# Kernel tuning notes

Measured on AMD Instinct MI355X. Metric: run time of the kernel, lower is better.

## Reference

```python
import jax, jax.numpy as jnp
import numpy as np

N_CELL = 400000
N_NET = 100000
E_PIN = 1600000
E2 = 400000
RAW_C = 8; RAW_N = 8; RAW_P = 8
HC = 64; HN = 64; HP = 16


def setup_inputs() -> dict:
    key = jax.random.key(0)
    ks = jax.random.split(key, 32)
    f32 = jnp.float32

    def lin(k, fan_in, fan_out):
        k1, k2 = jax.random.split(k)
        W = jax.random.normal(k1, (fan_in, fan_out), f32) / np.float32(np.sqrt(fan_in))
        b = jax.random.normal(k2, (fan_out,), f32) * 0.01
        return W, b

    inp = {}
    inp['cell_feat'] = jax.random.normal(ks[0], (N_CELL, RAW_C), f32)
    inp['net_feat'] = jax.random.normal(ks[1], (N_NET, RAW_N), f32)
    inp['pin_feat'] = jax.random.normal(ks[2], (E_PIN, RAW_P), f32)
    inp['cell_size'] = jax.random.uniform(ks[3], (N_CELL, 2), f32)
    inp['W_cell'], inp['b_cell'] = lin(ks[4], RAW_C + 2 * RAW_N, HC)
    inp['W_net'], inp['b_net'] = lin(ks[5], RAW_N + 2 * RAW_C, HN)
    inp['W_pin'], inp['b_pin'] = lin(ks[6], RAW_P, HP)
    inp['W_ew'], inp['b_ew'] = lin(ks[7], HP, 1)
    inp['W_self'] = jax.random.normal(ks[8], (HC, HC), f32) / np.float32(np.sqrt(HC))
    inp['W_neigh'] = jax.random.normal(ks[9], (HN, HC), f32) / np.float32(np.sqrt(HN))
    inp['b_sage'] = jax.random.normal(ks[10], (HC,), f32) * 0.01
    inp['W_dis'], inp['b_dis'] = lin(ks[11], 2 * HC + HN, 1)
    inp['W_def'], inp['b_def'] = lin(ks[12], 3 * HC + 2 * HN, 1)
    # 'pins' edges: cell -> net; 'pinned' is the reverse (net -> cell), same edge set
    inp['pins_src'] = jax.random.randint(ks[13], (E_PIN,), 0, N_CELL, jnp.int32)
    inp['pins_dst'] = jax.random.randint(ks[14], (E_PIN,), 0, N_NET, jnp.int32)
    # points-to family: all four etypes share the same 'fathers' ordering (asserted in torch)
    inp['fathers'] = jax.random.randint(ks[15], (E2,), 0, N_CELL, jnp.int32)
    inp['sons'] = jax.random.randint(ks[16], (E2,), 0, N_CELL, jnp.int32)
    inp['grandfathers'] = jax.random.randint(ks[17], (E2,), 0, N_CELL, jnp.int32)
    inp['fs_nets'] = jax.random.randint(ks[18], (E2,), 0, N_NET, jnp.int32)
    inp['gf_nets'] = jax.random.randint(ks[19], (E2,), 0, N_NET, jnp.int32)
    return inp


def _seg_mean_max(x, idx, n):
    # DGL fn.mean / fn.max semantics: zero-in-degree nodes get 0
    cnt = jax.ops.segment_sum(jnp.ones((idx.shape[0], 1), x.dtype), idx, num_segments=n)
    mean = jax.ops.segment_sum(x, idx, num_segments=n) / jnp.maximum(cnt, 1.0)
    mx = jax.ops.segment_max(x, idx, num_segments=n)
    mx = jnp.where(cnt > 0, mx, 0.0)
    return mean, mx, cnt


def reference(cell_feat, net_feat, pin_feat, cell_size,
              W_cell, b_cell, W_net, b_net, W_pin, b_pin, W_ew, b_ew,
              W_self, W_neigh, b_sage, W_dis, b_dis, W_def, b_def,
              pins_src, pins_dst, fathers, sons, grandfathers, fs_nets, gf_nets):
    n_cell = cell_feat.shape[0]
    n_net = net_feat.shape[0]
    # update_all over 'pins' (cell->net) and 'pinned' (net->cell): mean & max of src feats
    net_mean, net_max, _ = _seg_mean_max(cell_feat[pins_src], pins_dst, n_net)
    cell_mean, cell_max, cell_cnt = _seg_mean_max(net_feat[pins_dst], pins_src, n_cell)
    hc = jnp.tanh(jnp.concatenate([cell_feat, cell_mean, cell_max], axis=-1) @ W_cell + b_cell)
    hn = jnp.tanh(jnp.concatenate([net_feat, net_mean, net_max], axis=-1) @ W_net + b_net)
    hp = jnp.tanh(pin_feat @ W_pin + b_pin)
    # single pass: SAGEConv(mean) on 'pinned' with scalar edge weights
    ew = jnp.tanh(hp @ W_ew + b_ew)  # [E_PIN, 1]
    msg = hn[pins_dst] * ew          # src of 'pinned' edge = net
    h_neigh = jax.ops.segment_sum(msg, pins_src, num_segments=n_cell) / jnp.maximum(cell_cnt, 1.0)
    hidden_cell = hc @ W_self + h_neigh @ W_neigh + b_sage  # [N_CELL, HC]
    # gather-based edge readouts
    pair = jnp.concatenate([hidden_cell[fathers], hidden_cell[sons], hn[fs_nets]], axis=-1)
    ext = jnp.concatenate([hidden_cell[grandfathers], hidden_cell[fathers], hidden_cell[sons],
                           hn[gf_nets], hn[fs_nets]], axis=-1)
    edge_dis_ = jnp.exp(-2.0 + 15.0 * jnp.tanh(pair @ W_dis + b_dis)).reshape(-1)
    edge_deflect = jnp.tanh(ext @ W_def + b_def).reshape(-1) * (2.0 * jnp.pi)
    bound = (cell_size[fathers] + cell_size[sons]) * 0.5  # [E2, 2]
    edge_dis = edge_dis_ + jnp.min(bound, axis=1)
    return edge_dis, edge_deflect
```

## Files before the change

kernel.cpp:

```cpp
#include <hip/hip_runtime.h>
#include <math.h>

#define N_CELL 400000
#define N_NET  100000
#define E_PIN  1600000
#define E2     400000


__global__ void __launch_bounds__(256) k_hist(
    const int* __restrict__ src, const int* __restrict__ dst,
    int* __restrict__ cell_deg, int* __restrict__ net_deg)
{
    int e = blockIdx.x * 256 + threadIdx.x;
    if (e >= E_PIN) return;
    atomicAdd(&net_deg[dst[e]], 1);
    atomicAdd(&cell_deg[src[e]], 1);
}

__global__ void __launch_bounds__(256) k_alloc(
    const int* __restrict__ deg, int* __restrict__ ptr, int* __restrict__ cur,
    int* __restrict__ cursor, int n)
{
    __shared__ int s[256];
    __shared__ int base;
    int tid = threadIdx.x;
    int i = blockIdx.x * 256 + tid;
    int d = (i < n) ? deg[i] : 0;
    int v = d;
    s[tid] = v;
    __syncthreads();
    for (int o = 1; o < 256; o <<= 1) {
        int t = (tid >= o) ? s[tid - o] : 0;
        __syncthreads();
        v += t;
        s[tid] = v;
        __syncthreads();
    }
    if (tid == 255) base = atomicAdd(cursor, v);
    __syncthreads();
    if (i < n) {
        int p = base + v - d;
        ptr[i] = p;
        cur[i] = p;
    }
}

__global__ void __launch_bounds__(256) k_fill(
    const int* __restrict__ src, const int* __restrict__ dst,
    int* __restrict__ net_cur, int* __restrict__ cell_cur,
    int* __restrict__ csr_net_cell, int* __restrict__ csr_cell_net,
    int* __restrict__ edge_slot)
{
    int e = blockIdx.x * 256 + threadIdx.x;
    if (e >= E_PIN) return;
    int s = src[e], d = dst[e];
    int p = atomicAdd(&net_cur[d], 1);
    csr_net_cell[p] = s;
    int q = atomicAdd(&cell_cur[s], 1);
    csr_cell_net[q] = d;
    edge_slot[e] = q;
}

__global__ void __launch_bounds__(256) k_ew(
    const float* __restrict__ pin_feat,
    const float* __restrict__ W_pin, const float* __restrict__ b_pin,
    const float* __restrict__ W_ew, const float* __restrict__ b_ew,
    const int* __restrict__ edge_slot,
    float* __restrict__ ew_csr)
{
    __shared__ float Wp[8 * 16];
    __shared__ float bp[16];
    __shared__ float We[16];
    __shared__ float be_s;
    int tid = threadIdx.x;
    if (tid < 128) Wp[tid] = W_pin[tid];
    if (tid < 16) { bp[tid] = b_pin[tid]; We[tid] = W_ew[tid]; }
    if (tid == 0) be_s = b_ew[0];
    __syncthreads();
    int e = blockIdx.x * 256 + tid;
    if (e >= E_PIN) return;
    float p[8];
    #pragma unroll
    for (int k = 0; k < 8; ++k) p[k] = pin_feat[e * 8 + k];
    float acc = be_s;
    #pragma unroll
    for (int j = 0; j < 16; ++j) {
        float h = bp[j];
        #pragma unroll
        for (int k = 0; k < 8; ++k) h += p[k] * Wp[k * 16 + j];
        acc += tanhf(h) * We[j];
    }
    ew_csr[edge_slot[e]] = tanhf(acc);
}

__global__ void __launch_bounds__(256) k_net(
    const float* __restrict__ net_feat, const float* __restrict__ cell_feat,
    const int* __restrict__ net_ptr, const int* __restrict__ net_deg,
    const int* __restrict__ csr_cell,
    const float* __restrict__ W_net, const float* __restrict__ b_net,
    const float* __restrict__ W_neigh,
    const float* __restrict__ W_dis, const float* __restrict__ W_def,
    float* __restrict__ hnW, float* __restrict__ npack)
{
    __shared__ float smem[11648];
    float* xs24 = smem;
    float* Ws24 = smem + 1600;
    float* HN   = smem + 3136;
    float* Wn   = smem + 7296;
    float* Wd3  = smem + 11392;
    float* bs   = smem + 11584;

    int tid = threadIdx.x;
    int w = tid >> 6, l = tid & 63;
    int tile = blockIdx.x * 64;

    for (int i = tid; i < 1536; i += 256) Ws24[i] = W_net[i];
    for (int i = tid; i < 4096; i += 256) Wn[i] = W_neigh[i];
    if (tid < 192) Wd3[tid] = (tid < 64) ? W_dis[128 + tid] : W_def[128 + tid];
    if (tid < 64) bs[tid] = b_net[tid];

    int g = l >> 3, k = l & 7;
    #pragma unroll
    for (int p = 0; p < 2; ++p) {
        int rl = p * 32 + w * 8 + g;
        int row = tile + rl;
        int base = 0, deg = 0;
        if (row < N_NET) { base = net_ptr[row]; deg = net_deg[row]; }
        float sum = 0.0f, mx = -INFINITY;
        for (int j = 0; j < deg; ++j) {
            int idx = csr_cell[base + j];
            float v = cell_feat[idx * 8 + k];
            sum += v;
            mx = fmaxf(mx, v);
        }
        float inv = (deg > 0) ? 1.0f / (float)deg : 1.0f;
        float sf = (row < N_NET) ? net_feat[row * 8 + k] : 0.0f;
        xs24[rl * 25 + k] = sf;
        xs24[rl * 25 + 8 + k] = sum * inv;
        xs24[rl * 25 + 16 + k] = (deg > 0) ? mx : 0.0f;
    }
    __syncthreads();

    int rg = l >> 2, cc = l & 3, c0 = w * 16 + cc * 4;
    {
        float acc[4][4];
        #pragma unroll
        for (int i = 0; i < 4; ++i) {
            float4 b4 = *(const float4*)&bs[c0];
            acc[i][0] = b4.x; acc[i][1] = b4.y; acc[i][2] = b4.z; acc[i][3] = b4.w;
        }
        for (int kk = 0; kk < 24; ++kk) {
            float4 wv = *(const float4*)&Ws24[kk * 64 + c0];
            #pragma unroll
            for (int i = 0; i < 4; ++i) {
                float x = xs24[(rg * 4 + i) * 25 + kk];
                acc[i][0] += x * wv.x; acc[i][1] += x * wv.y;
                acc[i][2] += x * wv.z; acc[i][3] += x * wv.w;
            }
        }
        #pragma unroll
        for (int i = 0; i < 4; ++i)
            #pragma unroll
            for (int j = 0; j < 4; ++j)
                HN[(rg * 4 + i) * 65 + c0 + j] = tanhf(acc[i][j]);
    }
    __syncthreads();

    {
        float acc[4][4];
        #pragma unroll
        for (int i = 0; i < 4; ++i)
            #pragma unroll
            for (int j = 0; j < 4; ++j) acc[i][j] = 0.0f;
        for (int kk = 0; kk < 64; ++kk) {
            float4 wv = *(const float4*)&Wn[kk * 64 + c0];
            #pragma unroll
            for (int i = 0; i < 4; ++i) {
                float x = HN[(rg * 4 + i) * 65 + kk];
                acc[i][0] += x * wv.x; acc[i][1] += x * wv.y;
                acc[i][2] += x * wv.z; acc[i][3] += x * wv.w;
            }
        }
        #pragma unroll
        for (int i = 0; i < 4; ++i) {
            int row = tile + rg * 4 + i;
            if (row < N_NET)
                *(float4*)&hnW[(size_t)row * 64 + c0] =
                    make_float4(acc[i][0], acc[i][1], acc[i][2], acc[i][3]);
        }
    }

    {
        int row = tid & 63, d = tid >> 6;
        float a = 0.0f;
        if (d < 3)
            for (int kk = 0; kk < 64; ++kk) a += HN[row * 65 + kk] * Wd3[d * 64 + kk];
        int grow = tile + row;
        if (grow < N_NET) npack[(size_t)grow * 4 + d] = (d < 3) ? a : 0.0f;
    }
}

__global__ void __launch_bounds__(256) k_cell(
    const float* __restrict__ cell_feat, const float* __restrict__ net_feat,
    const float* __restrict__ cell_size,
    const int* __restrict__ cell_ptr, const int* __restrict__ cell_deg,
    const int* __restrict__ csr_net, const float* __restrict__ ew_csr,
    const float* __restrict__ hnW,
    const float* __restrict__ W_cell, const float* __restrict__ b_cell,
    const float* __restrict__ W_self, const float* __restrict__ b_sage,
    const float* __restrict__ W_dis, const float* __restrict__ W_def,
    float* __restrict__ cellpack)
{
    __shared__ float smem[12864];
    float* xs24 = smem;
    float* Ws24 = smem + 1600;
    float* XN   = smem;
    float* X    = smem + 4160;
    float* Wsf  = smem + 8320;
    float* Wd5  = smem + 12416;
    float* bs24 = smem + 12736;
    float* bsg  = smem + 12800;

    int tid = threadIdx.x;
    int w = tid >> 6, l = tid & 63;
    int tile = blockIdx.x * 64;

    for (int i = tid; i < 1536; i += 256) Ws24[i] = W_cell[i];
    for (int i = tid; i < 4096; i += 256) Wsf[i] = W_self[i];
    if (tid < 64) { bs24[tid] = b_cell[tid]; bsg[tid] = b_sage[tid]; }
    { int i = tid; if (i < 320) Wd5[i] = (i < 128) ? W_dis[i] : W_def[i - 128]; }

    int g = l >> 3, k = l & 7;
    float4 xa[2], xb[2];
    #pragma unroll
    for (int p = 0; p < 2; ++p) {
        int rl = p * 32 + w * 8 + g;
        int row = tile + rl;
        int base = cell_ptr[row], deg = cell_deg[row];
        float sum = 0.0f, mx = -INFINITY;
        float4 a0 = make_float4(0, 0, 0, 0), a1 = make_float4(0, 0, 0, 0);
        for (int j = 0; j < deg; ++j) {
            int slot = base + j;
            int net = csr_net[slot];
            float wt = ew_csr[slot];
            float v = net_feat[net * 8 + k];
            sum += v;
            mx = fmaxf(mx, v);
            const float4* hp = (const float4*)(hnW + (size_t)net * 64 + k * 8);
            float4 u = hp[0], u2 = hp[1];
            a0.x += wt * u.x;  a0.y += wt * u.y;  a0.z += wt * u.z;  a0.w += wt * u.w;
            a1.x += wt * u2.x; a1.y += wt * u2.y; a1.z += wt * u2.z; a1.w += wt * u2.w;
        }
        float inv = (deg > 0) ? 1.0f / (float)deg : 1.0f;
        xs24[rl * 25 + k] = cell_feat[row * 8 + k];
        xs24[rl * 25 + 8 + k] = sum * inv;
        xs24[rl * 25 + 16 + k] = (deg > 0) ? mx : 0.0f;
        xa[p] = make_float4(a0.x * inv, a0.y * inv, a0.z * inv, a0.w * inv);
        xb[p] = make_float4(a1.x * inv, a1.y * inv, a1.z * inv, a1.w * inv);
    }
    __syncthreads();

    int rg = l >> 2, cc = l & 3, c0 = w * 16 + cc * 4;
    {
        float acc[4][4];
        #pragma unroll
        for (int i = 0; i < 4; ++i) {
            float4 b4 = *(const float4*)&bs24[c0];
            acc[i][0] = b4.x; acc[i][1] = b4.y; acc[i][2] = b4.z; acc[i][3] = b4.w;
        }
        for (int kk = 0; kk < 24; ++kk) {
            float4 wv = *(const float4*)&Ws24[kk * 64 + c0];
            #pragma unroll
            for (int i = 0; i < 4; ++i) {
                float x = xs24[(rg * 4 + i) * 25 + kk];
                acc[i][0] += x * wv.x; acc[i][1] += x * wv.y;
                acc[i][2] += x * wv.z; acc[i][3] += x * wv.w;
            }
        }
        __syncthreads();
        #pragma unroll
        for (int i = 0; i < 4; ++i)
            #pragma unroll
            for (int j = 0; j < 4; ++j)
                X[(rg * 4 + i) * 65 + c0 + j] = tanhf(acc[i][j]);
    }
    #pragma unroll
    for (int p = 0; p < 2; ++p) {
        int rl = p * 32 + w * 8 + g;
        float* xn = &XN[rl * 65 + k * 8];
        xn[0] = xa[p].x; xn[1] = xa[p].y; xn[2] = xa[p].z; xn[3] = xa[p].w;
        xn[4] = xb[p].x; xn[5] = xb[p].y; xn[6] = xb[p].z; xn[7] = xb[p].w;
    }
    __syncthreads();

    {
        float acc[4][4];
        #pragma unroll
        for (int i = 0; i < 4; ++i) {
            float4 b4 = *(const float4*)&bsg[c0];
            int r = rg * 4 + i;
            acc[i][0] = b4.x + XN[r * 65 + c0];
            acc[i][1] = b4.y + XN[r * 65 + c0 + 1];
            acc[i][2] = b4.z + XN[r * 65 + c0 + 2];
            acc[i][3] = b4.w + XN[r * 65 + c0 + 3];
        }
        for (int kk = 0; kk < 64; ++kk) {
            float4 wv = *(const float4*)&Wsf[kk * 64 + c0];
            #pragma unroll
            for (int i = 0; i < 4; ++i) {
                float x = X[(rg * 4 + i) * 65 + kk];
                acc[i][0] += x * wv.x; acc[i][1] += x * wv.y;
                acc[i][2] += x * wv.z; acc[i][3] += x * wv.w;
            }
        }
        __syncthreads();
        #pragma unroll
        for (int i = 0; i < 4; ++i)
            #pragma unroll
            for (int j = 0; j < 4; ++j)
                X[(rg * 4 + i) * 65 + c0 + j] = acc[i][j];
    }
    __syncthreads();

    {
        int row = tid & 63, d = tid >> 6;
        float a = 0.0f, a2 = 0.0f;
        for (int kk = 0; kk < 64; ++kk) {
            float x = X[row * 65 + kk];
            a += x * Wd5[d * 64 + kk];
            if (d == 0) a2 += x * Wd5[256 + kk];
        }
        size_t gbase = (size_t)(tile + row) * 8;
        cellpack[gbase + d] = a;
        if (d == 0) cellpack[gbase + 4] = a2;
        else if (d == 1) cellpack[gbase + 5] = cell_size[(size_t)(tile + row) * 2];
        else if (d == 2) cellpack[gbase + 6] = cell_size[(size_t)(tile + row) * 2 + 1];
        else cellpack[gbase + 7] = 0.0f;
    }
}

__global__ void __launch_bounds__(256) k_edge(
    const float* __restrict__ cellpack, const float* __restrict__ npack,
    const int* __restrict__ fa, const int* __restrict__ so, const int* __restrict__ gf,
    const int* __restrict__ fsn, const int* __restrict__ gfn,
    const float* __restrict__ b_dis, const float* __restrict__ b_def,
    float* __restrict__ out)
{
    int e = blockIdx.x * 256 + threadIdx.x;
    if (e >= E2) return;
    int f = fa[e], s = so[e], g = gf[e], nf = fsn[e], ng = gfn[e];
    const float4* cf = (const float4*)(cellpack + (size_t)f * 8);
    float4 f0 = cf[0], f1 = cf[1];
    const float4* cs = (const float4*)(cellpack + (size_t)s * 8);
    float4 s0 = cs[0], s1 = cs[1];
    float g2 = cellpack[(size_t)g * 8 + 2];
    float4 n0 = *(const float4*)(npack + (size_t)nf * 4);
    float ng1 = npack[(size_t)ng * 4 + 1];
    float dis = f0.x + s0.y + n0.x + b_dis[0];
    float defl = g2 + f0.w + s1.x + ng1 + n0.z + b_def[0];
    float o1 = expf(-2.0f + 15.0f * tanhf(dis));
    float bx = (f1.y + s1.y) * 0.5f;
    float by = (f1.z + s1.z) * 0.5f;
    out[e] = o1 + fminf(bx, by);
    out[E2 + e] = tanhf(defl) * 6.28318530717958647692f;
}

extern "C" void kernel_launch(void* const* d_in, const int* in_sizes, int n_in,
                              void* d_out, int out_size, void* d_ws, size_t ws_size,
                              hipStream_t stream)
{
    const float* cell_feat = (const float*)d_in[0];
    const float* net_feat  = (const float*)d_in[1];
    const float* pin_feat  = (const float*)d_in[2];
    const float* cell_size = (const float*)d_in[3];
    const float* W_cell = (const float*)d_in[4];
    const float* b_cell = (const float*)d_in[5];
    const float* W_net  = (const float*)d_in[6];
    const float* b_net  = (const float*)d_in[7];
    const float* W_pin  = (const float*)d_in[8];
    const float* b_pin  = (const float*)d_in[9];
    const float* W_ew   = (const float*)d_in[10];
    const float* b_ew   = (const float*)d_in[11];
    const float* W_self = (const float*)d_in[12];
    const float* W_neigh= (const float*)d_in[13];
    const float* b_sage = (const float*)d_in[14];
    const float* W_dis  = (const float*)d_in[15];
    const float* b_dis  = (const float*)d_in[16];
    const float* W_def  = (const float*)d_in[17];
    const float* b_def  = (const float*)d_in[18];
    const int* pins_src = (const int*)d_in[19];
    const int* pins_dst = (const int*)d_in[20];
    const int* fathers  = (const int*)d_in[21];
    const int* sons     = (const int*)d_in[22];
    const int* grandf   = (const int*)d_in[23];
    const int* fs_nets  = (const int*)d_in[24];
    const int* gf_nets  = (const int*)d_in[25];

    char* ws = (char*)d_ws;
    size_t off = 0;
    auto alloc = [&](size_t bytes) -> void* {
        void* p = ws + off;
        off += (bytes + 255) & ~(size_t)255;
        return p;
    };
    int* cursors   = (int*)alloc(2 * 4);
    int* net_deg   = (int*)alloc((size_t)N_NET * 4);
    int* cell_deg  = (int*)alloc((size_t)N_CELL * 4);
    size_t zero_bytes = off;
    int* net_ptr   = (int*)alloc((size_t)N_NET * 4);
    int* net_cur   = (int*)alloc((size_t)N_NET * 4);
    int* cell_ptr  = (int*)alloc((size_t)N_CELL * 4);
    int* cell_cur  = (int*)alloc((size_t)N_CELL * 4);
    int* csr_net_cell = (int*)alloc((size_t)E_PIN * 4);
    int* csr_cell_net = (int*)alloc((size_t)E_PIN * 4);
    int* edge_slot    = (int*)alloc((size_t)E_PIN * 4);
    float* ew_csr   = (float*)alloc((size_t)E_PIN * 4);
    float* hnW      = (float*)alloc((size_t)N_NET * 64 * 4);
    float* npack    = (float*)alloc((size_t)N_NET * 4 * 4);
    float* cellpack = (float*)alloc((size_t)N_CELL * 8 * 4);
    if (off > ws_size) return;

    hipMemsetAsync(d_ws, 0, zero_bytes, stream);

    k_hist<<<(E_PIN + 255) / 256, 256, 0, stream>>>(pins_src, pins_dst, cell_deg, net_deg);
    k_alloc<<<(N_NET + 255) / 256, 256, 0, stream>>>(net_deg, net_ptr, net_cur, &cursors[0], N_NET);
    k_alloc<<<(N_CELL + 255) / 256, 256, 0, stream>>>(cell_deg, cell_ptr, cell_cur, &cursors[1], N_CELL);
    k_fill<<<(E_PIN + 255) / 256, 256, 0, stream>>>(
        pins_src, pins_dst, net_cur, cell_cur, csr_net_cell, csr_cell_net, edge_slot);

    k_ew<<<(E_PIN + 255) / 256, 256, 0, stream>>>(
        pin_feat, W_pin, b_pin, W_ew, b_ew, edge_slot, ew_csr);

    k_net<<<(N_NET + 63) / 64, 256, 0, stream>>>(
        net_feat, cell_feat, net_ptr, net_deg, csr_net_cell,
        W_net, b_net, W_neigh, W_dis, W_def, hnW, npack);

    k_cell<<<N_CELL / 64, 256, 0, stream>>>(
        cell_feat, net_feat, cell_size, cell_ptr, cell_deg, csr_cell_net, ew_csr,
        hnW, W_cell, b_cell, W_self, b_sage, W_dis, W_def, cellpack);

    k_edge<<<(E2 + 255) / 256, 256, 0, stream>>>(
        cellpack, npack, fathers, sons, grandf, fs_nets, gf_nets,
        b_dis, b_def, (float*)d_out);
}
```

Baseline: 1.056 ms.

## Fold SAGE weights into readout projections to shrink per-net gathered payload

Precomputes W_self·w_dis/def and W_neigh·w_dis/def in a small prep kernel, so hidden_cell is never materialized; cells only need 5 scalar projections. Nets now store 5 projected scalars (plus raw features) instead of a 64-wide hnW row, cutting the per-pin gather in k_cell from 64 floats to a few. Also unrolls neighbor gather loops by 4 and adds launch-bound occupancy hints. Relies on linearity of the SAGE layer, so floating-point summation order changes.

```diff
diff --git a/kernel.cpp b/kernel.cpp
--- a/kernel.cpp
+++ b/kernel.cpp
@@ -59,6 +59,41 @@
     int q = atomicAdd(&cell_cur[s], 1);
     csr_cell_net[q] = d;
     edge_slot[e] = q;
+}
+
+__global__ void __launch_bounds__(256) k_prep(
+    const float* __restrict__ Wself, const float* __restrict__ Wneigh,
+    const float* __restrict__ Wdis, const float* __restrict__ Wdef,
+    const float* __restrict__ bsage,
+    float* __restrict__ u_all, float* __restrict__ v_all, float* __restrict__ bsd)
+{
+    __shared__ float wd[5][64];
+    int tid = threadIdx.x;
+    if (tid < 320) {
+        int d = tid >> 6, i = tid & 63;
+        wd[d][i] = (d < 2) ? Wdis[d * 64 + i] : Wdef[(d - 2) * 64 + i];
+    }
+    __syncthreads();
+    for (int o = tid; o < 320; o += 256) {
+        int d = o >> 6, i = o & 63;
+        float a = 0.0f, bvec = 0.0f;
+        for (int j = 0; j < 64; ++j) {
+            a += Wself[i * 64 + j] * wd[d][j];
+            bvec += Wneigh[i * 64 + j] * wd[d][j];
+        }
+        u_all[o] = a;
+        v_all[o] = bvec;
+    }
+    if (tid < 64) {
+        v_all[5 * 64 + tid] = Wdis[128 + tid];
+        v_all[6 * 64 + tid] = Wdef[192 + tid];
+        v_all[7 * 64 + tid] = Wdef[256 + tid];
+    }
+    if (tid < 5) {
+        float a = 0.0f;
+        for (int j = 0; j < 64; ++j) a += bsage[j] * wd[tid][j];
+        bsd[tid] = a;
+    }
 }
 
 __global__ void __launch_bounds__(256) k_ew(
@@ -93,30 +128,26 @@
     ew_csr[edge_slot[e]] = tanhf(acc);
 }
 
-__global__ void __launch_bounds__(256) k_net(
+__global__ void __launch_bounds__(256, 4) k_net(
     const float* __restrict__ net_feat, const float* __restrict__ cell_feat,
     const int* __restrict__ net_ptr, const int* __restrict__ net_deg,
     const int* __restrict__ csr_cell,
     const float* __restrict__ W_net, const float* __restrict__ b_net,
-    const float* __restrict__ W_neigh,
-    const float* __restrict__ W_dis, const float* __restrict__ W_def,
-    float* __restrict__ hnW, float* __restrict__ npack)
-{
-    __shared__ float smem[11648];
-    float* xs24 = smem;
-    float* Ws24 = smem + 1600;
-    float* HN   = smem + 3136;
-    float* Wn   = smem + 7296;
-    float* Wd3  = smem + 11392;
-    float* bs   = smem + 11584;
+    const float* __restrict__ v_all,
+    float* __restrict__ netpack)
+{
+    __shared__ float xs24[64 * 25];
+    __shared__ float Ws24[24 * 64];
+    __shared__ float HN[64 * 68];
+    __shared__ float V8[8 * 64];
+    __shared__ float bs[64];
 
     int tid = threadIdx.x;
     int w = tid >> 6, l = tid & 63;
     int tile = blockIdx.x * 64;
 
     for (int i = tid; i < 1536; i += 256) Ws24[i] = W_net[i];
-    for (int i = tid; i < 4096; i += 256) Wn[i] = W_neigh[i];
-    if (tid < 192) Wd3[tid] = (tid < 64) ? W_dis[128 + tid] : W_def[128 + tid];
+    for (int i = tid; i < 512; i += 256) V8[i] = v_all[i];
     if (tid < 64) bs[tid] = b_net[tid];
 
     int g = l >> 3, k = l & 7;
@@ -127,9 +158,19 @@
         int base = 0, deg = 0;
         if (row < N_NET) { base = net_ptr[row]; deg = net_deg[row]; }
         float sum = 0.0f, mx = -INFINITY;
-        for (int j = 0; j < deg; ++j) {
-            int idx = csr_cell[base + j];
-            float v = cell_feat[idx * 8 + k];
+        int j = 0;
+        for (; j + 4 <= deg; j += 4) {
+            int i0 = csr_cell[base + j], i1 = csr_cell[base + j + 1];
+            int i2 = csr_cell[base + j + 2], i3 = csr_cell[base + j + 3];
+            float v0 = cell_feat[i0 * 8 + k];
+            float v1 = cell_feat[i1 * 8 + k];
+            float v2 = cell_feat[i2 * 8 + k];
+            float v3 = cell_feat[i3 * 8 + k];
+            sum += (v0 + v1) + (v2 + v3);
+            mx = fmaxf(fmaxf(fmaxf(mx, v0), fmaxf(v1, v2)), v3);
+        }
+        for (; j < deg; ++j) {
+            float v = cell_feat[csr_cell[base + j] * 8 + k];
             sum += v;
             mx = fmaxf(mx, v);
         }
@@ -138,15 +179,16 @@
         xs24[rl * 25 + k] = sf;
         xs24[rl * 25 + 8 + k] = sum * inv;
         xs24[rl * 25 + 16 + k] = (deg > 0) ? mx : 0.0f;
-    }
-    __syncthreads();
-
-    int rg = l >> 2, cc = l & 3, c0 = w * 16 + cc * 4;
+        if (row < N_NET) netpack[(size_t)row * 16 + k] = sf;
+    }
+    __syncthreads();
+
     {
+        int rg = l >> 2, cc = l & 3, c0 = w * 16 + cc * 4;
         float acc[4][4];
+        float4 b4 = *(const float4*)&bs[c0];
         #pragma unroll
         for (int i = 0; i < 4; ++i) {
-            float4 b4 = *(const float4*)&bs[c0];
             acc[i][0] = b4.x; acc[i][1] = b4.y; acc[i][2] = b4.z; acc[i][3] = b4.w;
         }
         for (int kk = 0; kk < 24; ++kk) {
@@ -160,112 +202,99 @@
         }
         #pragma unroll
         for (int i = 0; i < 4; ++i)
-            #pragma unroll
-            for (int j = 0; j < 4; ++j)
-                HN[(rg * 4 + i) * 65 + c0 + j] = tanhf(acc[i][j]);
-    }
-    __syncthreads();
-
-    {
-        float acc[4][4];
-        #pragma unroll
-        for (int i = 0; i < 4; ++i)
-            #pragma unroll
-            for (int j = 0; j < 4; ++j) acc[i][j] = 0.0f;
-        for (int kk = 0; kk < 64; ++kk) {
-            float4 wv = *(const float4*)&Wn[kk * 64 + c0];
-            #pragma unroll
-            for (int i = 0; i < 4; ++i) {
-                float x = HN[(rg * 4 + i) * 65 + kk];
-                acc[i][0] += x * wv.x; acc[i][1] += x * wv.y;
-                acc[i][2] += x * wv.z; acc[i][3] += x * wv.w;
-            }
-        }
-        #pragma unroll
-        for (int i = 0; i < 4; ++i) {
-            int row = tile + rg * 4 + i;
-            if (row < N_NET)
-                *(float4*)&hnW[(size_t)row * 64 + c0] =
-                    make_float4(acc[i][0], acc[i][1], acc[i][2], acc[i][3]);
-        }
-    }
-
-    {
-        int row = tid & 63, d = tid >> 6;
+            *(float4*)&HN[(rg * 4 + i) * 68 + c0] =
+                make_float4(tanhf(acc[i][0]), tanhf(acc[i][1]),
+                            tanhf(acc[i][2]), tanhf(acc[i][3]));
+    }
+    __syncthreads();
+
+    #pragma unroll
+    for (int pass = 0; pass < 2; ++pass) {
+        int d = (tid >> 6) + pass * 4;
+        int row = tid & 63;
         float a = 0.0f;
-        if (d < 3)
-            for (int kk = 0; kk < 64; ++kk) a += HN[row * 65 + kk] * Wd3[d * 64 + kk];
+        for (int t = 0; t < 64; ++t) {
+            int kk = (row + t) & 63;
+            a += HN[row * 68 + kk] * V8[d * 64 + kk];
+        }
         int grow = tile + row;
-        if (grow < N_NET) npack[(size_t)grow * 4 + d] = (d < 3) ? a : 0.0f;
-    }
-}
-
-__global__ void __launch_bounds__(256) k_cell(
-    const float* __restrict__ cell_feat, const float* __restrict__ net_feat,
-    const float* __restrict__ cell_size,
+        if (grow < N_NET) netpack[(size_t)grow * 16 + 8 + d] = a;
+    }
+}
+
+__global__ void __launch_bounds__(256, 4) k_cell(
+    const float* __restrict__ cell_feat, const float* __restrict__ cell_size,
     const int* __restrict__ cell_ptr, const int* __restrict__ cell_deg,
     const int* __restrict__ csr_net, const float* __restrict__ ew_csr,
-    const float* __restrict__ hnW,
+    const float* __restrict__ netpack,
     const float* __restrict__ W_cell, const float* __restrict__ b_cell,
-    const float* __restrict__ W_self, const float* __restrict__ b_sage,
-    const float* __restrict__ W_dis, const float* __restrict__ W_def,
+    const float* __restrict__ u_all, const float* __restrict__ bsd,
     float* __restrict__ cellpack)
 {
-    __shared__ float smem[12864];
-    float* xs24 = smem;
-    float* Ws24 = smem + 1600;
-    float* XN   = smem;
-    float* X    = smem + 4160;
-    float* Wsf  = smem + 8320;
-    float* Wd5  = smem + 12416;
-    float* bs24 = smem + 12736;
-    float* bsg  = smem + 12800;
+    __shared__ float xs24[64 * 25];
+    __shared__ float Ws24[24 * 64];
+    __shared__ float HC[64 * 68];
+    __shared__ float U5[5 * 64];
+    __shared__ float MS[64 * 9];
+    __shared__ float bs[64];
 
     int tid = threadIdx.x;
     int w = tid >> 6, l = tid & 63;
     int tile = blockIdx.x * 64;
 
     for (int i = tid; i < 1536; i += 256) Ws24[i] = W_cell[i];
-    for (int i = tid; i < 4096; i += 256) Wsf[i] = W_self[i];
-    if (tid < 64) { bs24[tid] = b_cell[tid]; bsg[tid] = b_sage[tid]; }
-    { int i = tid; if (i < 320) Wd5[i] = (i < 128) ? W_dis[i] : W_def[i - 128]; }
+    for (int i = tid; i < 320; i += 256) U5[i] = u_all[i];
+    if (tid < 64) bs[tid] = b_cell[tid];
 
     int g = l >> 3, k = l & 7;
-    float4 xa[2], xb[2];
     #pragma unroll
     for (int p = 0; p < 2; ++p) {
         int rl = p * 32 + w * 8 + g;
         int row = tile + rl;
         int base = cell_ptr[row], deg = cell_deg[row];
-        float sum = 0.0f, mx = -INFINITY;
-        float4 a0 = make_float4(0, 0, 0, 0), a1 = make_float4(0, 0, 0, 0);
-        for (int j = 0; j < deg; ++j) {
+        float sum = 0.0f, mx = -INFINITY, sacc = 0.0f;
+        int j = 0;
+        for (; j + 4 <= deg; j += 4) {
             int slot = base + j;
-            int net = csr_net[slot];
+            int n0 = csr_net[slot], n1 = csr_net[slot + 1];
+            int n2 = csr_net[slot + 2], n3 = csr_net[slot + 3];
+            float w0 = ew_csr[slot], w1 = ew_csr[slot + 1];
+            float w2 = ew_csr[slot + 2], w3 = ew_csr[slot + 3];
+            float f0 = netpack[(size_t)n0 * 16 + k];
+            float f1 = netpack[(size_t)n1 * 16 + k];
+            float f2 = netpack[(size_t)n2 * 16 + k];
+            float f3 = netpack[(size_t)n3 * 16 + k];
+            float s0 = netpack[(size_t)n0 * 16 + 8 + k];
+            float s1 = netpack[(size_t)n1 * 16 + 8 + k];
+            float s2 = netpack[(size_t)n2 * 16 + 8 + k];
+            float s3 = netpack[(size_t)n3 * 16 + 8 + k];
+            sum += (f0 + f1) + (f2 + f3);
+            mx = fmaxf(fmaxf(fmaxf(mx, f0), fmaxf(f1, f2)), f3);
+            sacc += (w0 * s0 + w1 * s1) + (w2 * s2 + w3 * s3);
+        }
+        for (; j < deg; ++j) {
+            int slot = base + j;
+            int n = csr_net[slot];
             float wt = ew_csr[slot];
-            float v = net_feat[net * 8 + k];
-            sum += v;
-            mx = fmaxf(mx, v);
-            const float4* hp = (const float4*)(hnW + (size_t)net * 64 + k * 8);
-            float4 u = hp[0], u2 = hp[1];
-            a0.x += wt * u.x;  a0.y += wt * u.y;  a0.z += wt * u.z;  a0.w += wt * u.w;
-            a1.x += wt * u2.x; a1.y += wt * u2.y; a1.z += wt * u2.z; a1.w += wt * u2.w;
+            float f = netpack[(size_t)n * 16 + k];
+            sum += f;
+            mx = fmaxf(mx, f);
+            sacc += wt * netpack[(size_t)n * 16 + 8 + k];
         }
         float inv = (deg > 0) ? 1.0f / (float)deg : 1.0f;
         xs24[rl * 25 + k] = cell_feat[row * 8 + k];
         xs24[rl * 25 + 8 + k] = sum * inv;
         xs24[rl * 25 + 16 + k] = (deg > 0) ? mx : 0.0f;
-        xa[p] = make_float4(a0.x * inv, a0.y * inv, a0.z * inv, a0.w * inv);
-        xb[p] = make_float4(a1.x * inv, a1.y * inv, a1.z * inv, a1.w * inv);
-    }
-    __syncthreads();
-
-    int rg = l >> 2, cc = l & 3, c0 = w * 16 + cc * 4;
+        MS[rl * 9 + k] = sacc * inv;
+    }
+    __syncthreads();
+
     {
+        int rg = l >> 2, cc = l & 3, c0 = w * 16 + cc * 4;
         float acc[4][4];
+        float4 b4 = *(const float4*)&bs[c0];
         #pragma unroll
         for (int i = 0; i < 4; ++i) {
-            float4 b4 = *(const float4*)&bs24[c0];
             acc[i][0] = b4.x; acc[i][1] = b4.y; acc[i][2] = b4.z; acc[i][3] = b4.w;
         }
         for (int kk = 0; kk < 24; ++kk) {
@@ -277,70 +306,48 @@
                 acc[i][2] += x * wv.z; acc[i][3] += x * wv.w;
             }
         }
-        __syncthreads();
         #pragma unroll
         for (int i = 0; i < 4; ++i)
-            #pragma unroll
-            for (int j = 0; j < 4; ++j)
-                X[(rg * 4 + i) * 65 + c0 + j] = tanhf(acc[i][j]);
-    }
-    #pragma unroll
-    for (int p = 0; p < 2; ++p) {
-        int rl = p * 32 + w * 8 + g;
-        float* xn = &XN[rl * 65 + k * 8];
-        xn[0] = xa[p].x; xn[1] = xa[p].y; xn[2] = xa[p].z; xn[3] = xa[p].w;
-        xn[4] = xb[p].x; xn[5] = xb[p].y; xn[6] = xb[p].z; xn[7] = xb[p].w;
+            *(float4*)&HC[(rg * 4 + i) * 68 + c0] =
+                make_float4(tanhf(acc[i][0]), tanhf(acc[i][1]),
+                            tanhf(acc[i][2]), tanhf(acc[i][3]));
     }
     __syncthreads();
 
     {
-        float acc[4][4];
-        #pragma unroll
-        for (int i = 0; i < 4; ++i) {
-            float4 b4 = *(const float4*)&bsg[c0];
-            int r = rg * 4 + i;
-            acc[i][0] = b4.x + XN[r * 65 + c0];
-            acc[i][1] = b4.y + XN[r * 65 + c0 + 1];
-            acc[i][2] = b4.z + XN[r * 65 + c0 + 2];
-            acc[i][3] = b4.w + XN[r * 65 + c0 + 3];
-        }
-        for (int kk = 0; kk < 64; ++kk) {
-            float4 wv = *(const float4*)&Wsf[kk * 64 + c0];
-            #pragma unroll
-            for (int i = 0; i < 4; ++i) {
-                float x = X[(rg * 4 + i) * 65 + kk];
-                acc[i][0] += x * wv.x; acc[i][1] += x * wv.y;
-                acc[i][2] += x * wv.z; acc[i][3] += x * wv.w;
+        int d = tid >> 6;
+        int row = tid & 63;
+        float a = 0.0f;
+        for (int t = 0; t < 64; ++t) {
+            int kk = (row + t) & 63;
+            a += HC[row * 68 + kk] * U5[d * 64 + kk];
+        }
+        size_t gbase = (size_t)(tile + row) * 8;
+        cellpack[gbase + d] = a + MS[row * 9 + d] + bsd[d];
+    }
+    {
+        int d = tid >> 6;
+        int row = tid & 63;
+        size_t gbase = (size_t)(tile + row) * 8;
+        if (d == 0) {
+            float a = 0.0f;
+            for (int t = 0; t < 64; ++t) {
+                int kk = (row + t) & 63;
+                a += HC[row * 68 + kk] * U5[4 * 64 + kk];
             }
-        }
-        __syncthreads();
-        #pragma unroll
-        for (int i = 0; i < 4; ++i)
-            #pragma unroll
-            for (int j = 0; j < 4; ++j)
-                X[(rg * 4 + i) * 65 + c0 + j] = acc[i][j];
-    }
-    __syncthreads();
-
-    {
-        int row = tid & 63, d = tid >> 6;
-        float a = 0.0f, a2 = 0.0f;
-        for (int kk = 0; kk < 64; ++kk) {
-            float x = X[row * 65 + kk];
-            a += x * Wd5[d * 64 + kk];
-            if (d == 0) a2 += x * Wd5[256 + kk];
-        }
-        size_t gbase = (size_t)(tile + row) * 8;
-        cellpack[gbase + d] = a;
-        if (d == 0) cellpack[gbase + 4] = a2;
-        else if (d == 1) cellpack[gbase + 5] = cell_size[(size_t)(tile + row) * 2];
-        else if (d == 2) cellpack[gbase + 6] = cell_size[(size_t)(tile + row) * 2 + 1];
-        else cellpack[gbase + 7] = 0.0f;
+            cellpack[gbase + 4] = a + MS[row * 9 + 4] + bsd[4];
+        } else if (d == 1) {
+            cellpack[gbase + 5] = cell_size[(size_t)(tile + row) * 2];
+        } else if (d == 2) {
+            cellpack[gbase + 6] = cell_size[(size_t)(tile + row) * 2 + 1];
+        } else {
+            cellpack[gbase + 7] = 0.0f;
+        }
     }
 }
 
 __global__ void __launch_bounds__(256) k_edge(
-    const float* __restrict__ cellpack, const float* __restrict__ npack,
+    const float* __restrict__ cellpack, const float* __restrict__ netpack,
     const int* __restrict__ fa, const int* __restrict__ so, const int* __restrict__ gf,
     const int* __restrict__ fsn, const int* __restrict__ gfn,
     const float* __restrict__ b_dis, const float* __restrict__ b_def,
@@ -354,10 +361,10 @@
     const float4* cs = (const float4*)(cellpack + (size_t)s * 8);
     float4 s0 = cs[0], s1 = cs[1];
     float g2 = cellpack[(size_t)g * 8 + 2];
-    float4 n0 = *(const float4*)(npack + (size_t)nf * 4);
-    float ng1 = npack[(size_t)ng * 4 + 1];
-    float dis = f0.x + s0.y + n0.x + b_dis[0];
-    float defl = g2 + f0.w + s1.x + ng1 + n0.z + b_def[0];
+    float4 nfp = *(const float4*)(netpack + (size_t)nf * 16 + 12);
+    float ng_t = netpack[(size_t)ng * 16 + 14];
+    float dis = f0.x + s0.y + nfp.y + b_dis[0];
+    float defl = g2 + f0.w + s1.x + ng_t + nfp.w + b_def[0];
     float o1 = expf(-2.0f + 15.0f * tanhf(dis));
     float bx = (f1.y + s1.y) * 0.5f;
     float by = (f1.z + s1.z) * 0.5f;
@@ -415,12 +422,17 @@
     int* csr_cell_net = (int*)alloc((size_t)E_PIN * 4);
     int* edge_slot    = (int*)alloc((size_t)E_PIN * 4);
     float* ew_csr   = (float*)alloc((size_t)E_PIN * 4);
-    float* hnW      = (float*)alloc((size_t)N_NET * 64 * 4);
-    float* npack    = (float*)alloc((size_t)N_NET * 4 * 4);
+    float* netpack  = (float*)alloc((size_t)N_NET * 16 * 4);
     float* cellpack = (float*)alloc((size_t)N_CELL * 8 * 4);
+    float* u_all    = (float*)alloc(5 * 64 * 4);
+    float* v_all    = (float*)alloc(8 * 64 * 4);
+    float* bsd      = (float*)alloc(8 * 4);
     if (off > ws_size) return;
 
     hipMemsetAsync(d_ws, 0, zero_bytes, stream);
+
+    k_prep<<<1, 256, 0, stream>>>(W_self, W_neigh, W_dis, W_def, b_sage,
+                                  u_all, v_all, bsd);
 
     k_hist<<<(E_PIN + 255) / 256, 256, 0, stream>>>(pins_src, pins_dst, cell_deg, net_deg);
     k_alloc<<<(N_NET + 255) / 256, 256, 0, stream>>>(net_deg, net_ptr, net_cur, &cursors[0], N_NET);
@@ -433,13 +445,13 @@
 
     k_net<<<(N_NET + 63) / 64, 256, 0, stream>>>(
         net_feat, cell_feat, net_ptr, net_deg, csr_net_cell,
-        W_net, b_net, W_neigh, W_dis, W_def, hnW, npack);
+        W_net, b_net, v_all, netpack);
 
     k_cell<<<N_CELL / 64, 256, 0, stream>>>(
-        cell_feat, net_feat, cell_size, cell_ptr, cell_deg, csr_cell_net, ew_csr,
-        hnW, W_cell, b_cell, W_self, b_sage, W_dis, W_def, cellpack);
+        cell_feat, cell_size, cell_ptr, cell_deg, csr_cell_net, ew_csr,
+        netpack, W_cell, b_cell, u_all, bsd, cellpack);
 
     k_edge<<<(E2 + 255) / 256, 256, 0, stream>>>(
-        cellpack, npack, fathers, sons, grandf, fs_nets, gf_nets,
+        cellpack, netpack, fathers, sons, grandf, fs_nets, gf_nets,
         b_dis, b_def, (float*)d_out);
 }
```

Measured after the change: 1.543 ms. 46.1% more time.
